# Optimization experiments

Hardware: AMD Instinct MI355X
Metric: run time of the kernel (lower is better)

Reference implementation:

```python
import jax, jax.numpy as jnp
import numpy as np

VOCAB, D_MODEL, MAX_LEN = 32000, 1024, 4096
B, S = 4, 2048


def make_pe(max_len, d_model):
    pos = np.arange(max_len)[:, None].astype(np.float32)
    div = np.exp(np.arange(0, d_model, 2).astype(np.float32) * -(np.log(10000.0) / d_model))
    pe = np.zeros((max_len, d_model), dtype=np.float32)
    pe[:, 0::2] = np.sin(pos * div)
    pe[:, 1::2] = np.cos(pos * div)
    return jnp.asarray(pe)


def setup_inputs() -> dict:
    key = jax.random.key(0)
    k1, k2, k3 = jax.random.split(key, 3)
    text = jax.random.randint(k1, (B, S), 0, VOCAB)
    W = jax.random.normal(k2, (D_MODEL, VOCAB), dtype=jnp.float32) * 0.02
    b = jax.random.normal(k3, (D_MODEL,), dtype=jnp.float32) * 0.02
    pe = make_pe(MAX_LEN, D_MODEL)
    return {"text": text, "W": W, "b": b, "pe": pe}


def reference(text, W, b, pe):
    # one_hot(text) @ W.T + b  ==  gather of W columns: out[b,s,:] = W[:, text[b,s]] + b
    emb = jnp.take(W.T, text, axis=0)          # [B, S, d_model]
    out = emb + b + pe[: text.shape[-1]]       # positional add, broadcast over batch
    return out  # dropout is identity in eval mode
```

## Files before the change

### kernel.cpp

```cpp
#include <hip/hip_runtime.h>


#define VOCAB  32000
#define DMODEL 1024
#define S_LEN  2048
#define B_N    4
#define NTOK   (B_N * S_LEN)
#define VT     128
#define DT     64
#define NBIN   (VOCAB / VT)
#define NDT    (DMODEL / DT)
#define NBLK   (NBIN * NDT)
#define LSTRIDE (VT + 1)

__global__ __launch_bounds__(1024) void bin_k(const int* __restrict__ text,
                                              int2* __restrict__ sorted,
                                              int* __restrict__ tile_off) {
    __shared__ int cnt[256];
    __shared__ int scn[256];
    const int t = threadIdx.x;
    if (t < 256) cnt[t] = 0;
    __syncthreads();

    int toks[8];
    #pragma unroll
    for (int j = 0; j < 8; ++j) {
        toks[j] = text[t * 8 + j];
        atomicAdd(&cnt[toks[j] >> 7], 1);
    }
    __syncthreads();

    if (t < 256) scn[t] = cnt[t];
    __syncthreads();
    for (int off = 1; off < 256; off <<= 1) {
        int x = 0;
        if (t < 256 && t >= off) x = scn[t - off];
        __syncthreads();
        if (t < 256) scn[t] += x;
        __syncthreads();
    }
    if (t < 256) {
        const int start = scn[t] - cnt[t];
        tile_off[t] = start;
        cnt[t] = start;
    }
    __syncthreads();

    #pragma unroll
    for (int j = 0; j < 8; ++j) {
        const int tok = toks[j];
        const int slot = atomicAdd(&cnt[tok >> 7], 1);
        sorted[slot] = make_int2(tok, t * 8 + j);
    }
}

__global__ __launch_bounds__(256) void gather_k(const int2* __restrict__ sorted,
                                                const int* __restrict__ tile_off,
                                                const float* __restrict__ W,
                                                const float* __restrict__ bias,
                                                const float* __restrict__ pe,
                                                float* __restrict__ out) {
    __shared__ float lds[DT * LSTRIDE];

    const int bid = blockIdx.x;
    const int vt = bid >> 4;
    const int dt = bid & (NDT - 1);
    const int v0 = vt * VT;
    const int d0 = dt * DT;
    const int t  = threadIdx.x;

    {
        const int c4 = t & 31;
        const int r0 = t >> 5;
        #pragma unroll
        for (int i = 0; i < 8; ++i) {
            const int row = r0 + i * 8;
            const float4 w4 = *reinterpret_cast<const float4*>(
                W + (size_t)(d0 + row) * VOCAB + v0 + c4 * 4);
            float* lp = lds + row * LSTRIDE + c4 * 4;
            lp[0] = w4.x; lp[1] = w4.y; lp[2] = w4.z; lp[3] = w4.w;
        }
    }
    __syncthreads();

    const int a0 = tile_off[vt];
    const int a1 = tile_off[vt + 1];
    const int lane = t & 63;
    const int wv   = t >> 6;
    const float bv = bias[d0 + lane];

    for (int i = a0 + wv; i < a1; i += 4) {
        const int2 p = sorted[i];
        const int tokl = p.x - v0;
        const int bs   = p.y;
        const int s    = bs & (S_LEN - 1);
        const float wval = lds[lane * LSTRIDE + tokl];
        const float pv = pe[(size_t)s * DMODEL + d0 + lane];
        out[(size_t)bs * DMODEL + d0 + lane] = wval + bv + pv;
    }
}

__global__ __launch_bounds__(256) void embed_pe_direct(const int* __restrict__ text,
                                                       const float* __restrict__ W,
                                                       const float* __restrict__ bias,
                                                       const float* __restrict__ pe,
                                                       float* __restrict__ out) {
    const int bs = blockIdx.x;
    const int s  = bs & (S_LEN - 1);
    const int tok = text[bs];
    const int d = threadIdx.x << 2;
    const float4 b4 = *reinterpret_cast<const float4*>(bias + d);
    const float4 p4 = *reinterpret_cast<const float4*>(pe + (size_t)s * DMODEL + d);
    const float* wcol = W + (size_t)d * VOCAB + tok;
    float4 o;
    o.x = wcol[0]                 + b4.x + p4.x;
    o.y = wcol[(size_t)VOCAB]     + b4.y + p4.y;
    o.z = wcol[(size_t)2 * VOCAB] + b4.z + p4.z;
    o.w = wcol[(size_t)3 * VOCAB] + b4.w + p4.w;
    *reinterpret_cast<float4*>(out + (size_t)bs * DMODEL + d) = o;
}

extern "C" void kernel_launch(void* const* d_in, const int* in_sizes, int n_in,
                              void* d_out, int out_size, void* d_ws, size_t ws_size,
                              hipStream_t stream) {
    const int*   text = (const int*)d_in[0];
    const float* W    = (const float*)d_in[1];
    const float* bias = (const float*)d_in[2];
    const float* pe   = (const float*)d_in[3];
    float*       out  = (float*)d_out;

    const size_t sorted_bytes = (size_t)NTOK * sizeof(int2);
    const size_t off_bytes    = 257 * sizeof(int);
    if (ws_size < sorted_bytes + off_bytes) {
        embed_pe_direct<<<NTOK, 256, 0, stream>>>(text, W, bias, pe, out);
        return;
    }

    int2* sorted   = (int2*)d_ws;
    int*  tile_off = (int*)((char*)d_ws + sorted_bytes);

    bin_k   <<<1, 1024, 0, stream>>>(text, sorted, tile_off);
    gather_k<<<NBLK, 256, 0, stream>>>(sorted, tile_off, W, bias, pe, out);
}
```

Measured before the change: 42.72 us.

## Process groups of vocab tiles per block with double-buffered LDS prefetch

Each gather block now walks a group of eight vocab tiles over a narrower 32-wide d_model slice. The next tile's W slice is prefetched into registers while the current tile's tokens are processed, then written to the alternate LDS buffer. Each wave handles two tokens at a time with half-waves. This hides the W tile load latency and cuts the block count. The cost is less parallelism (fewer blocks), serial work per block, and only 128-byte contiguous output writes per token.

```diff
diff --git a/kernel.cpp b/kernel.cpp
--- a/kernel.cpp
+++ b/kernel.cpp
@@ -7,10 +7,12 @@
 #define B_N    4
 #define NTOK   (B_N * S_LEN)
 #define VT     128
-#define DT     64
+#define DT     32
 #define NBIN   (VOCAB / VT)
 #define NDT    (DMODEL / DT)
-#define NBLK   (NBIN * NDT)
+#define GRP    8
+#define NVG    ((NBIN + GRP - 1) / GRP)
+#define NBLK   (NDT * NVG)
 #define LSTRIDE (VT + 1)
 
 __global__ __launch_bounds__(1024) void bin_k(const int* __restrict__ text,
@@ -60,43 +62,66 @@
                                                 const float* __restrict__ bias,
                                                 const float* __restrict__ pe,
                                                 float* __restrict__ out) {
-    __shared__ float lds[DT * LSTRIDE];
+    __shared__ float lds[2][DT][LSTRIDE];
 
     const int bid = blockIdx.x;
-    const int vt = bid >> 4;
     const int dt = bid & (NDT - 1);
-    const int v0 = vt * VT;
+    const int vg = bid >> 5;
     const int d0 = dt * DT;
     const int t  = threadIdx.x;
 
-    {
-        const int c4 = t & 31;
-        const int r0 = t >> 5;
-        #pragma unroll
-        for (int i = 0; i < 8; ++i) {
-            const int row = r0 + i * 8;
-            const float4 w4 = *reinterpret_cast<const float4*>(
-                W + (size_t)(d0 + row) * VOCAB + v0 + c4 * 4);
-            float* lp = lds + row * LSTRIDE + c4 * 4;
-            lp[0] = w4.x; lp[1] = w4.y; lp[2] = w4.z; lp[3] = w4.w;
-        }
-    }
-    __syncthreads();
+    const int c4 = t & 31;
+    const int r0 = t >> 5;
 
-    const int a0 = tile_off[vt];
-    const int a1 = tile_off[vt + 1];
     const int lane = t & 63;
     const int wv   = t >> 6;
-    const float bv = bias[d0 + lane];
+    const int half = lane >> 5;
+    const int dl   = lane & 31;
+    const float bv = bias[d0 + dl];
 
-    for (int i = a0 + wv; i < a1; i += 4) {
-        const int2 p = sorted[i];
-        const int tokl = p.x - v0;
-        const int bs   = p.y;
-        const int s    = bs & (S_LEN - 1);
-        const float wval = lds[lane * LSTRIDE + tokl];
-        const float pv = pe[(size_t)s * DMODEL + d0 + lane];
-        out[(size_t)bs * DMODEL + d0 + lane] = wval + bv + pv;
+    const int vt_begin = vg * GRP;
+    const int vt_end   = (vt_begin + GRP < NBIN) ? vt_begin + GRP : NBIN;
+    const int ntile    = vt_end - vt_begin;
+
+    float4 r[4];
+
+    auto stage_regs = [&](int vt) {
+        const float* wp = W + (size_t)(d0 + r0) * VOCAB + vt * VT + c4 * 4;
+        #pragma unroll
+        for (int i = 0; i < 4; ++i)
+            r[i] = *reinterpret_cast<const float4*>(wp + (size_t)(8 * i) * VOCAB);
+    };
+    auto write_lds = [&](int buf) {
+        #pragma unroll
+        for (int i = 0; i < 4; ++i) {
+            float* lp = &lds[buf][r0 + 8 * i][c4 * 4];
+            lp[0] = r[i].x; lp[1] = r[i].y; lp[2] = r[i].z; lp[3] = r[i].w;
+        }
+    };
+
+    stage_regs(vt_begin);
+    write_lds(0);
+
+    for (int g = 0; g < ntile; ++g) {
+        if (g + 1 < ntile) stage_regs(vt_begin + g + 1);
+        __syncthreads();
+
+        const int vt = vt_begin + g;
+        const int v0 = vt * VT;
+        const int a0 = tile_off[vt];
+        const int a1 = tile_off[vt + 1];
+        const float* ldsb = &lds[g & 1][0][0];
+
+        for (int i = a0 + wv * 2 + half; i < a1; i += 8) {
+            const int2 p = sorted[i];
+            const int tokl = p.x - v0;
+            const int bs   = p.y;
+            const int s    = bs & (S_LEN - 1);
+            const float wval = ldsb[dl * LSTRIDE + tokl];
+            const float pv = pe[(size_t)s * DMODEL + d0 + dl];
+            out[(size_t)bs * DMODEL + d0 + dl] = wval + bv + pv;
+        }
+        if (g + 1 < ntile) write_lds((g + 1) & 1);
     }
 }
 
```

New measurement: 45.19 us. 1.06x slower.
